# Optimization experiments

Hardware: AMD Instinct MI355X
Metric: run time of the kernel (lower is better)

## Reference

```python
import jax, jax.numpy as jnp
import numpy as np

B, S, H = 4, 2048, 1024
E, K, F = 8, 2, 4096


def setup_inputs() -> dict:
    key = jax.random.key(0)
    ks = jax.random.split(key, 6)
    x = jax.random.normal(ks[0], (B, S, H), dtype=jnp.float32)
    gate_w = jax.random.normal(ks[1], (H, E), dtype=jnp.float32) * 0.02
    w1 = jax.random.normal(ks[2], (E, H, F), dtype=jnp.float32) * 0.02
    b1 = jnp.zeros((E, F), dtype=jnp.float32)
    w2 = jax.random.normal(ks[3], (E, F, H), dtype=jnp.float32) * 0.02
    b2 = jnp.zeros((E, H), dtype=jnp.float32)
    return {"x": x, "gate_w": gate_w, "w1": w1, "b1": b1, "w2": w2, "b2": b2}


def reference(x, gate_w, w1, b1, w2, b2):
    # NOTE: the torch module masks expert inputs per token, but since each
    # expert's output is re-masked by the same mask, the math is exactly
    # out[t] = sum_i renorm_prob[t,i] * expert_{topk_idx[t,i]}(x[t]).
    # Dropout is identity in eval mode.
    T = B * S
    x_flat = x.reshape(T, H)

    gate_scores = x_flat @ gate_w                      # [T, E]
    gate_probs = jax.nn.softmax(gate_scores, axis=-1)  # [T, E]
    topk_vals, topk_idx = jax.lax.top_k(gate_probs, K)  # [T, K]
    topk_w = jax.nn.softmax(topk_vals, axis=-1)        # renormalize via softmax (as in source)

    # Combine weights per (token, expert): sum over top-k slots.
    onehot = jax.nn.one_hot(topk_idx, E, dtype=x.dtype)           # [T, K, E]
    comb = jnp.einsum('tk,tke->te', topk_w, onehot)               # [T, E]

    # Run all experts densely (faithful to naive module; combine masks out unrouted).
    h = jnp.einsum('th,ehf->etf', x_flat, w1) + b1[:, None, :]    # [E, T, F]
    h = jax.nn.relu(h)
    expert_out = jnp.einsum('etf,efh->eth', h, w2) + b2[:, None, :]  # [E, T, H]

    out_flat = jnp.einsum('te,eth->th', comb, expert_out)         # [T, H]
    output = out_flat.reshape(B, S, H)

    # Load-balance loss: KL(uniform || softmax(mean gate prob)), batchmean over E.
    expert_usage = gate_probs.mean(axis=0)                        # [E]
    log_sm = jax.nn.log_softmax(expert_usage, axis=0)
    uniform = jnp.full((E,), 1.0 / E, dtype=x.dtype)
    kl = jnp.sum(uniform * (jnp.log(uniform) - log_sm)) / E
    load_balance_loss = 0.01 * kl
    return output, load_balance_loss
```

## Files before the change

kernel.cpp:

```cpp
#include <hip/hip_runtime.h>
#include <stdint.h>

#define T_TOK 8192
#define HD 1024
#define NE 8
#define FD 4096
#define RALLOC 18432
#define G1 1152
#define G2 384
#define NKT1 16
#define GATE_BLOCKS 1024

typedef __attribute__((ext_vector_type(8))) short bf16x8;
typedef __attribute__((ext_vector_type(4))) float f32x4;
typedef __attribute__((ext_vector_type(4))) short s16x4;

__device__ __forceinline__ unsigned short f2bf(float f) {
  unsigned u = __builtin_bit_cast(unsigned, f);
  u += 0x7fffu + ((u >> 16) & 1u);
  return (unsigned short)(u >> 16);
}

__device__ __forceinline__ void gld_lds16(const void* g, void* l) {
  __builtin_amdgcn_global_load_lds(
      (const __attribute__((address_space(1))) void*)g,
      (__attribute__((address_space(3))) void*)l, 16, 0, 0);
}

__global__ __launch_bounds__(256) void k_transpose2(const float* __restrict__ w1,
                                                    const float* __restrict__ w2,
                                                    unsigned short* __restrict__ w1t,
                                                    unsigned short* __restrict__ w2t) {
  __shared__ unsigned short tile[64 * 80];
  const int i = blockIdx.x;
  const float* src;
  unsigned short* dst;
  int R, C, r0, c0;
  if (i < 8192) {
    const int e = i >> 10, rem = i & 1023;
    R = HD; C = FD; r0 = (rem >> 6) << 6; c0 = (rem & 63) << 6;
    src = w1 + (size_t)e * R * C; dst = w1t + (size_t)e * R * C;
  } else {
    const int e = (i - 8192) >> 10, rem = (i - 8192) & 1023;
    R = FD; C = HD; r0 = (rem >> 4) << 6; c0 = (rem & 15) << 6;
    src = w2 + (size_t)e * R * C; dst = w2t + (size_t)e * R * C;
  }
  const int tid = threadIdx.x;
  {
    const int r = tid >> 2, cg = (tid & 3) * 16;
    #pragma unroll
    for (int m = 0; m < 4; ++m) {
      float4 v = *(const float4*)(src + (size_t)(r0 + r) * C + c0 + cg + 4 * m);
      s16x4 pv;
      pv[0] = (short)f2bf(v.x); pv[1] = (short)f2bf(v.y);
      pv[2] = (short)f2bf(v.z); pv[3] = (short)f2bf(v.w);
      *(s16x4*)&tile[r * 80 + cg + 4 * m] = pv;
    }
  }
  __syncthreads();
  {
    const int c = tid >> 2, rg = (tid & 3) * 16;
    bf16x8 v0, v1;
    #pragma unroll
    for (int j = 0; j < 8; ++j) v0[j] = (short)tile[(rg + j) * 80 + c];
    #pragma unroll
    for (int j = 0; j < 8; ++j) v1[j] = (short)tile[(rg + 8 + j) * 80 + c];
    unsigned short* dp = dst + (size_t)(c0 + c) * R + r0 + rg;
    *(bf16x8*)dp = v0;
    *(bf16x8*)(dp + 8) = v1;
  }
}

__global__ __launch_bounds__(512) void k_gating(const float* __restrict__ x,
                                                const float* __restrict__ gw,
                                                int* __restrict__ toke,
                                                float* __restrict__ tokw,
                                                int* __restrict__ counts8,
                                                double* __restrict__ part,
                                                unsigned short* __restrict__ xbf) {
  __shared__ float gwT[8 * 1024];
  __shared__ double sp[8][8];
  __shared__ int scnt[8];
  const int tid = threadIdx.x;
  const int lane = tid & 63;
  const int w = tid >> 6;
  if (tid < 8) scnt[tid] = 0;
  #pragma unroll
  for (int rep = 0; rep < 16; ++rep) {
    int idx = rep * 512 + tid;
    gwT[(idx & 7) * 1024 + (idx >> 3)] = gw[idx];
  }
  __syncthreads();

  const int t = blockIdx.x * 8 + w;
  double acc[8];
  #pragma unroll
  for (int e = 0; e < 8; ++e) acc[e] = 0.0;
  const float* xr = x + (size_t)t * HD;
  unsigned short* xbr = xbf + (size_t)t * HD;
  #pragma unroll
  for (int j = 0; j < 4; ++j) {
    const int hh = j * 256 + lane * 4;
    float4 xv = *(const float4*)(xr + hh);
    s16x4 pv;
    pv[0] = (short)f2bf(xv.x); pv[1] = (short)f2bf(xv.y);
    pv[2] = (short)f2bf(xv.z); pv[3] = (short)f2bf(xv.w);
    *(s16x4*)(xbr + hh) = pv;
    #pragma unroll
    for (int e = 0; e < 8; ++e) {
      float4 gv = *(const float4*)(gwT + e * 1024 + hh);
      acc[e] += (double)xv.x * (double)gv.x;
      acc[e] += (double)xv.y * (double)gv.y;
      acc[e] += (double)xv.z * (double)gv.z;
      acc[e] += (double)xv.w * (double)gv.w;
    }
  }
  for (int off = 32; off > 0; off >>= 1) {
    #pragma unroll
    for (int e = 0; e < 8; ++e) acc[e] += __shfl_xor(acc[e], off, 64);
  }
  double m = acc[0];
  #pragma unroll
  for (int e = 1; e < 8; ++e) m = fmax(m, acc[e]);
  double p[8], ssum = 0.0;
  #pragma unroll
  for (int e = 0; e < 8; ++e) { p[e] = exp(acc[e] - m); ssum += p[e]; }
  double inv = 1.0 / ssum;
  #pragma unroll
  for (int e = 0; e < 8; ++e) p[e] *= inv;
  int e0 = 0;
  #pragma unroll
  for (int e = 1; e < 8; ++e) if (p[e] > p[e0]) e0 = e;
  int e1 = (e0 == 0) ? 1 : 0;
  #pragma unroll
  for (int e = 0; e < 8; ++e) if (e != e0 && p[e] > p[e1]) e1 = e;
  if (lane == 0) {
    double z = exp(p[e1] - p[e0]);
    double w0 = 1.0 / (1.0 + z);
    toke[2 * t] = e0; toke[2 * t + 1] = e1;
    tokw[2 * t] = (float)w0; tokw[2 * t + 1] = (float)(z / (1.0 + z));
    atomicAdd(&scnt[e0], 1);
    atomicAdd(&scnt[e1], 1);
    #pragma unroll
    for (int e = 0; e < 8; ++e) sp[w][e] = p[e];
  }
  __syncthreads();
  if (tid < 8) {
    double s = 0.0;
    #pragma unroll
    for (int q = 0; q < 8; ++q) s += sp[q][tid];
    part[(size_t)blockIdx.x * 8 + tid] = s;
    counts8[(size_t)blockIdx.x * 8 + tid] = scnt[tid];
  }
}

__global__ __launch_bounds__(256) void k_scan(const int* __restrict__ counts8,
                                              int* __restrict__ offs,
                                              int* __restrict__ cursors,
                                              const double* __restrict__ part,
                                              float* __restrict__ loss_out,
                                              int* __restrict__ rowmap,
                                              float* __restrict__ roww) {
  __shared__ double su[8];
  __shared__ int soffs[9];
  __shared__ int scnt[8];
  const int tid = threadIdx.x;
  const int e = tid >> 5, sub = tid & 31;
  double s = 0.0;
  int c = 0;
  for (int b = sub; b < GATE_BLOCKS; b += 32) {
    s += part[(size_t)b * 8 + e];
    c += counts8[(size_t)b * 8 + e];
  }
  for (int off = 16; off > 0; off >>= 1) {
    s += __shfl_xor(s, off, 64);
    c += __shfl_xor(c, off, 64);
  }
  if (sub == 0) { su[e] = s; scnt[e] = c; }
  __syncthreads();
  if (tid == 0) {
    int o = 0;
    for (int i = 0; i < 8; ++i) {
      soffs[i] = o; offs[i] = o; cursors[i * 16] = o;
      o += ((scnt[i] + 255) >> 8) << 8;
    }
    soffs[8] = o; offs[8] = o;
    double u[8], mx = -1e300;
    for (int i = 0; i < 8; ++i) { u[i] = su[i] / 8192.0; mx = fmax(mx, u[i]); }
    double se = 0.0;
    for (int i = 0; i < 8; ++i) se += exp(u[i] - mx);
    double lse = mx + log(se);
    double kl = 0.0;
    const double lu = log(0.125);
    for (int i = 0; i < 8; ++i) kl += 0.125 * (lu - (u[i] - lse));
    kl /= 8.0;
    loss_out[0] = (float)(0.01 * kl);
  }
  __syncthreads();
  for (int i = 0; i < 8; ++i) {
    int s0 = soffs[i] + scnt[i];
    int en = soffs[i + 1];
    for (int k = s0 + tid; k < en; k += 256) { rowmap[k] = 2 * T_TOK; roww[k] = 0.f; }
  }
}

__global__ __launch_bounds__(256) void k_scatter(const int* __restrict__ toke,
                                                 const float* __restrict__ tokw,
                                                 int* __restrict__ cursors,
                                                 int* __restrict__ rowmap,
                                                 float* __restrict__ roww) {
  const int t = blockIdx.x * 256 + threadIdx.x;
  const int lane = threadIdx.x & 63;
  #pragma unroll
  for (int k = 0; k < 2; ++k) {
    int e = toke[2 * t + k];
    float wv = tokw[2 * t + k];
    for (int ex = 0; ex < 8; ++ex) {
      unsigned long long mask = __ballot(e == ex);
      if (e == ex) {
        int leader = __ffsll((unsigned long long)mask) - 1;
        int rank = __popcll(mask & ((1ull << lane) - 1ull));
        int base = 0;
        if (lane == leader) base = atomicAdd(&cursors[ex * 16], __popcll(mask));
        base = __shfl(base, leader, 64);
        rowmap[base + rank] = 2 * t + k;
        roww[base + rank] = wv;
      }
    }
  }
}

#define RDA(buf, mh) do { _Pragma("unroll") for (int m_ = 0; m_ < 4; ++m_) { \
  af[m_][0] = *(const bf16x8*)(lds + (buf) * 65536 + wmOff + (mh) * 8192 + aoff[m_][0]); \
  af[m_][1] = *(const bf16x8*)(lds + (buf) * 65536 + wmOff + (mh) * 8192 + aoff[m_][1]); } } while (0)

#define RDB(buf, nh, B) do { _Pragma("unroll") for (int nf_ = 0; nf_ < 2; ++nf_) { \
  B[nf_][0] = *(const bf16x8*)(lds + (buf) * 65536 + wnOff + (nh) * 4096 + boff[nf_][0]); \
  B[nf_][1] = *(const bf16x8*)(lds + (buf) * 65536 + wnOff + (nh) * 4096 + boff[nf_][1]); } } while (0)

#define MMA(mh, nh, B) do { _Pragma("unroll") for (int m_ = 0; m_ < 4; ++m_) \
  _Pragma("unroll") for (int nf_ = 0; nf_ < 2; ++nf_) \
  _Pragma("unroll") for (int kh_ = 0; kh_ < 2; ++kh_) \
    acc[(mh) * 4 + m_][(nh) * 2 + nf_] = __builtin_amdgcn_mfma_f32_16x16x32_bf16( \
        af[m_][kh_], B[nf_][kh_], acc[(mh) * 4 + m_][(nh) * 2 + nf_], 0, 0, 0); } while (0)

#define SYNC_PRE() do { __builtin_amdgcn_sched_barrier(0); __builtin_amdgcn_s_barrier(); \
  asm volatile("s_waitcnt lgkmcnt(0)" ::: "memory"); __builtin_amdgcn_sched_barrier(0); \
  __builtin_amdgcn_s_setprio(1); } while (0)

#define SYNC_POST() do { __builtin_amdgcn_s_setprio(0); __builtin_amdgcn_sched_barrier(0); \
  __builtin_amdgcn_s_barrier(); __builtin_amdgcn_sched_barrier(0); } while (0)

#define SYNC_POST_VM() do { __builtin_amdgcn_s_setprio(0); __builtin_amdgcn_sched_barrier(0); \
  asm volatile("s_waitcnt vmcnt(4)" ::: "memory"); __builtin_amdgcn_sched_barrier(0); \
  __builtin_amdgcn_s_barrier(); __builtin_amdgcn_sched_barrier(0); } while (0)

#define FRAG_OFFSETS256() \
  int aoff[4][2], boff[2][2]; \
  { \
    const int kg = (lane >> 4) << 4; \
    _Pragma("unroll") \
    for (int m = 0; m < 4; ++m) { \
      int r = m * 16 + (lane & 15); \
      _Pragma("unroll") \
      for (int kh = 0; kh < 2; ++kh) \
        aoff[m][kh] = r * 128 + ((kh * 64 + kg) ^ ((r & 7) << 4)); \
    } \
    _Pragma("unroll") \
    for (int nf = 0; nf < 2; ++nf) { \
      int r = (wn & 1) * 64 + nf * 16 + (lane & 15); \
      _Pragma("unroll") \
      for (int kh = 0; kh < 2; ++kh) \
        boff[nf][kh] = r * 128 + ((kh * 64 + kg) ^ ((r & 7) << 4)); \
    } \
  }

__global__ __launch_bounds__(512, 2) void k_gemm1(const unsigned short* __restrict__ xbf,
                                                  const unsigned short* __restrict__ w1t,
                                                  const float* __restrict__ b1,
                                                  const int* __restrict__ rowmap,
                                                  const int* __restrict__ offs,
                                                  unsigned short* __restrict__ hbuf) {
  __shared__ char lds[131072];
  const int id = blockIdx.x;
  const int xcd = id & 7, l = id >> 3;
  const int ntr = offs[8] >> 8;
  const int nj = ntr * 16;
  const int q = nj >> 3, r8 = nj & 7;
  const int cnt = q + (xcd < r8 ? 1 : 0);
  if (l >= cnt) return;
  const int start = (xcd < r8) ? xcd * (q + 1) : r8 * (q + 1) + (xcd - r8) * q;
  const int g = start + l;
  const int rt = g >> 4, nb = g & 15;
  const int row0 = rt * 256;
  int e = 0;
  #pragma unroll
  for (int i = 1; i < 8; ++i) if (row0 >= offs[i]) e = i;
  const int n0 = nb * 256;
  const int tid = threadIdx.x;
  const int lane = tid & 63;
  const int wid = tid >> 6;
  const int wm = wid >> 2, wn = wid & 3;

  const int rl = tid >> 3;
  const int cbs = ((tid & 7) << 4) ^ ((rl & 7) << 4);
  const char* pA[2][2];
  #pragma unroll
  for (int h = 0; h < 2; ++h)
    #pragma unroll
    for (int l2 = 0; l2 < 2; ++l2) {
      int tok = rowmap[row0 + h * 128 + l2 * 64 + rl] >> 1;
      pA[h][l2] = (const char*)xbf + (size_t)tok * 2048 + cbs;
    }
  const char* pB00 = (const char*)w1t + (size_t)e * ((size_t)FD * HD * 2) +
                     (size_t)(n0 + rl) * 2048 + cbs;
  const int stw = wid * 1024;

#define STA1(buf, h, kt) do { \
  gld_lds16(pA[h][0] + (size_t)(kt) * 128, lds + (buf) * 65536 + (h) * 16384 + stw); \
  gld_lds16(pA[h][1] + (size_t)(kt) * 128, lds + (buf) * 65536 + (h) * 16384 + 8192 + stw); } while (0)
#define STB1(buf, h, kt) do { \
  gld_lds16(pB00 + (size_t)(h) * 128 * 2048 + (size_t)(kt) * 128, \
            lds + (buf) * 65536 + 32768 + (h) * 16384 + stw); \
  gld_lds16(pB00 + ((size_t)(h) * 128 + 64) * 2048 + (size_t)(kt) * 128, \
            lds + (buf) * 65536 + 32768 + (h) * 16384 + 8192 + stw); } while (0)

  FRAG_OFFSETS256();
  const int wmOff = wm * 16384;
  const int wnOff = 32768 + (wn >> 1) * 16384;

  f32x4 acc[8][4];
  #pragma unroll
  for (int a = 0; a < 8; ++a)
    #pragma unroll
    for (int b = 0; b < 4; ++b) acc[a][b] = (f32x4){0.f, 0.f, 0.f, 0.f};
  bf16x8 af[4][2], b0r[2][2], b1r[2][2];

  STA1(0, 0, 0); STA1(0, 1, 0); STB1(0, 0, 0); STB1(0, 1, 0);
  STB1(1, 0, 1); STB1(1, 1, 1);
  asm volatile("s_waitcnt vmcnt(4)" ::: "memory");
  __builtin_amdgcn_sched_barrier(0);
  __builtin_amdgcn_s_barrier();
  __builtin_amdgcn_sched_barrier(0);

  #pragma unroll 1
  for (int i = 0; i < NKT1 / 2; ++i) {
    const int k1 = 2 * i + 1, k2 = 2 * i + 2, k3 = 2 * i + 3;
    RDA(0, 0); RDB(0, 0, b0r); STA1(1, 0, k1); SYNC_PRE(); MMA(0, 0, b0r); SYNC_POST();
    RDB(0, 1, b1r);            STA1(1, 1, k1); SYNC_PRE(); MMA(0, 1, b1r); SYNC_POST();
    RDA(0, 1);                 STB1(0, 0, k2); SYNC_PRE(); MMA(1, 1, b1r); SYNC_POST();
                               STB1(0, 1, k2); SYNC_PRE(); MMA(1, 0, b0r); SYNC_POST_VM();
    RDA(1, 0); RDB(1, 0, b0r); STA1(0, 0, k2); SYNC_PRE(); MMA(0, 0, b0r); SYNC_POST();
    RDB(1, 1, b1r);            STA1(0, 1, k2); SYNC_PRE(); MMA(0, 1, b1r); SYNC_POST();
    RDA(1, 1);                 STB1(1, 0, k3); SYNC_PRE(); MMA(1, 1, b1r); SYNC_POST();
                               STB1(1, 1, k3); SYNC_PRE(); MMA(1, 0, b0r); SYNC_POST_VM();
  }

  asm volatile("s_waitcnt vmcnt(0)" ::: "memory");
  __builtin_amdgcn_sched_barrier(0);
  __syncthreads();
  #pragma unroll
  for (int na = 0; na < 4; ++na) {
    int c = wn * 64 + (na >> 1) * 32 + (na & 1) * 16 + (lane & 15);
    float bias = b1[(size_t)e * FD + n0 + c];
    #pragma unroll
    for (int ma = 0; ma < 8; ++ma) {
      #pragma unroll
      for (int j2 = 0; j2 < 4; ++j2) {
        int r = wm * 128 + (ma >> 2) * 64 + (ma & 3) * 16 + ((lane >> 4) << 2) + j2;
        float v = fmaxf(acc[ma][na][j2] + bias, 0.f);
        *(unsigned short*)(lds + r * 512 + ((c * 2) ^ ((r & 7) << 4))) = f2bf(v);
      }
    }
  }
  __syncthreads();
  #pragma unroll
  for (int s = 0; s < 16; ++s) {
    int flat = s * 512 + tid;
    int r = flat >> 5, ch = flat & 31;
    bf16x8 v = *(const bf16x8*)(lds + r * 512 + ((ch * 16) ^ ((r & 7) << 4)));
    *(bf16x8*)((char*)hbuf + (size_t)(row0 + r) * 8192 + (size_t)n0 * 2 + ch * 16) = v;
  }
#undef STA1
#undef STB1
}

__global__ __launch_bounds__(512, 2) void k_gemm2(const unsigned short* __restrict__ hbuf,
                                                  const unsigned short* __restrict__ w2t,
                                                  const float* __restrict__ b2,
                                                  const int* __restrict__ rowmap,
                                                  const float* __restrict__ roww,
                                                  const int* __restrict__ offs,
                                                  float* __restrict__ out2,
                                                  float* __restrict__ psplit) {
  __shared__ char lds[131072];
  const int id = blockIdx.x;
  int bx, by, kt0, niter, jj = -1;
  if (id < 256) {
    const int sid = (id & 7) * 32 + (id >> 3);
    bx = sid & 3; by = sid >> 2;
    kt0 = 0; niter = 32;
  } else {
    const int jid = id - 256;
    const int q = (jid & 7) * 16 + (jid >> 3);
    const int t = 256 + (q >> 2);
    const int nT2 = (offs[8] >> 8) * 4;
    if (t >= nT2) return;
    bx = t & 3; by = t >> 2;
    kt0 = (q & 3) * 16; niter = 8;
    jj = q;
  }
  const int row0 = by * 256;
  int e = 0;
  #pragma unroll
  for (int i = 1; i < 8; ++i) if (row0 >= offs[i]) e = i;
  const int n0 = bx * 256;
  const int tid = threadIdx.x;
  const int lane = tid & 63;
  const int wid = tid >> 6;
  const int wm = wid >> 2, wn = wid & 3;

  const int rl = tid >> 3;
  const int cbs = ((tid & 7) << 4) ^ ((rl & 7) << 4);
  const char* pA00 = (const char*)hbuf + (size_t)(row0 + rl) * 8192 + cbs;
  const char* pB00 = (const char*)w2t + (size_t)e * ((size_t)HD * FD * 2) +
                     (size_t)(n0 + rl) * 8192 + cbs;
  const int stw = wid * 1024;

#define STA2(buf, h, kt) do { \
  gld_lds16(pA00 + (size_t)(h) * 128 * 8192 + (size_t)(kt) * 128, \
            lds + (buf) * 65536 + (h) * 16384 + stw); \
  gld_lds16(pA00 + ((size_t)(h) * 128 + 64) * 8192 + (size_t)(kt) * 128, \
            lds + (buf) * 65536 + (h) * 16384 + 8192 + stw); } while (0)
#define STB2(buf, h, kt) do { \
  gld_lds16(pB00 + (size_t)(h) * 128 * 8192 + (size_t)(kt) * 128, \
            lds + (buf) * 65536 + 32768 + (h) * 16384 + stw); \
  gld_lds16(pB00 + ((size_t)(h) * 128 + 64) * 8192 + (size_t)(kt) * 128, \
            lds + (buf) * 65536 + 32768 + (h) * 16384 + 8192 + stw); } while (0)

  FRAG_OFFSETS256();
  const int wmOff = wm * 16384;
  const int wnOff = 32768 + (wn >> 1) * 16384;

  f32x4 acc[8][4];
  #pragma unroll
  for (int a = 0; a < 8; ++a)
    #pragma unroll
    for (int b = 0; b < 4; ++b) acc[a][b] = (f32x4){0.f, 0.f, 0.f, 0.f};
  bf16x8 af[4][2], b0r[2][2], b1r[2][2];

  STA2(0, 0, kt0); STA2(0, 1, kt0); STB2(0, 0, kt0); STB2(0, 1, kt0);
  STB2(1, 0, kt0 + 1); STB2(1, 1, kt0 + 1);
  asm volatile("s_waitcnt vmcnt(4)" ::: "memory");
  __builtin_amdgcn_sched_barrier(0);
  __builtin_amdgcn_s_barrier();
  __builtin_amdgcn_sched_barrier(0);

  #pragma unroll 1
  for (int i = 0; i < niter; ++i) {
    const int k1 = kt0 + 2 * i + 1, k2 = kt0 + 2 * i + 2, k3 = kt0 + 2 * i + 3;
    RDA(0, 0); RDB(0, 0, b0r); STA2(1, 0, k1); SYNC_PRE(); MMA(0, 0, b0r); SYNC_POST();
    RDB(0, 1, b1r);            STA2(1, 1, k1); SYNC_PRE(); MMA(0, 1, b1r); SYNC_POST();
    RDA(0, 1);                 STB2(0, 0, k2); SYNC_PRE(); MMA(1, 1, b1r); SYNC_POST();
                               STB2(0, 1, k2); SYNC_PRE(); MMA(1, 0, b0r); SYNC_POST_VM();
    RDA(1, 0); RDB(1, 0, b0r); STA2(0, 0, k2); SYNC_PRE(); MMA(0, 0, b0r); SYNC_POST();
    RDB(1, 1, b1r);            STA2(0, 1, k2); SYNC_PRE(); MMA(0, 1, b1r); SYNC_POST();
    RDA(1, 1);                 STB2(1, 0, k3); SYNC_PRE(); MMA(1, 1, b1r); SYNC_POST();
                               STB2(1, 1, k3); SYNC_PRE(); MMA(1, 0, b0r); SYNC_POST_VM();
  }

  asm volatile("s_waitcnt vmcnt(0)" ::: "memory");
  __builtin_amdgcn_sched_barrier(0);
  if (jj < 0) {
    #pragma unroll
    for (int ma = 0; ma < 8; ++ma) {
      #pragma unroll
      for (int j2 = 0; j2 < 4; ++j2) {
        int r = wm * 128 + (ma >> 2) * 64 + (ma & 3) * 16 + ((lane >> 4) << 2) + j2;
        int rm = rowmap[row0 + r];
        float wr = roww[row0 + r];
        float* orow = out2 + (size_t)rm * 1024 + n0;
        #pragma unroll
        for (int na = 0; na < 4; ++na) {
          int c = wn * 64 + (na >> 1) * 32 + (na & 1) * 16 + (lane & 15);
          orow[c] = (acc[ma][na][j2] + b2[(size_t)e * HD + n0 + c]) * wr;
        }
      }
    }
  } else {
    float* ps = psplit + (size_t)jj * 65536;
    #pragma unroll
    for (int ma = 0; ma < 8; ++ma) {
      #pragma unroll
      for (int j2 = 0; j2 < 4; ++j2) {
        int r = wm * 128 + (ma >> 2) * 64 + (ma & 3) * 16 + ((lane >> 4) << 2) + j2;
        #pragma unroll
        for (int na = 0; na < 4; ++na) {
          int c = wn * 64 + (na >> 1) * 32 + (na & 1) * 16 + (lane & 15);
          ps[r * 256 + c] = acc[ma][na][j2];
        }
      }
    }
  }
#undef STA2
#undef STB2
}

__global__ __launch_bounds__(512) void k_fix2(const float* __restrict__ psplit,
                                              const int* __restrict__ offs,
                                              const float* __restrict__ b2,
                                              const int* __restrict__ rowmap,
                                              const float* __restrict__ roww,
                                              float* __restrict__ out2) {
  const int nT2 = (offs[8] >> 8) * 4;
  const int t = 256 + blockIdx.x;
  if (t >= nT2) return;
  const int by = t >> 2, bx = t & 3;
  const int row0 = by * 256, n0 = bx * 256;
  int e = 0;
  #pragma unroll
  for (int i = 1; i < 8; ++i) if (row0 >= offs[i]) e = i;
  const float* ps = psplit + (size_t)blockIdx.x * 4 * 65536;
  const int cg = (threadIdx.x & 63) * 4;
  const int r0t = threadIdx.x >> 6;
  float4 bb = *(const float4*)(b2 + (size_t)e * HD + n0 + cg);
  for (int rr = 0; rr < 32; ++rr) {
    int r = rr * 8 + r0t;
    int rm = rowmap[row0 + r];
    float wr = roww[row0 + r];
    float4 s0 = *(const float4*)(ps + 0 * 65536 + r * 256 + cg);
    float4 s1 = *(const float4*)(ps + 1 * 65536 + r * 256 + cg);
    float4 s2 = *(const float4*)(ps + 2 * 65536 + r * 256 + cg);
    float4 s3 = *(const float4*)(ps + 3 * 65536 + r * 256 + cg);
    float4 o;
    o.x = wr * (s0.x + s1.x + s2.x + s3.x + bb.x);
    o.y = wr * (s0.y + s1.y + s2.y + s3.y + bb.y);
    o.z = wr * (s0.z + s1.z + s2.z + s3.z + bb.z);
    o.w = wr * (s0.w + s1.w + s2.w + s3.w + bb.w);
    *(float4*)(out2 + (size_t)rm * 1024 + n0 + cg) = o;
  }
}

__global__ __launch_bounds__(256) void k_combine(const float* __restrict__ out2,
                                                 float* __restrict__ out) {
  const int t = blockIdx.x;
  const int i = threadIdx.x * 4;
  float4 a = *(const float4*)(out2 + (size_t)(2 * t) * 1024 + i);
  float4 b = *(const float4*)(out2 + (size_t)(2 * t + 1) * 1024 + i);
  float4 r;
  r.x = a.x + b.x; r.y = a.y + b.y; r.z = a.z + b.z; r.w = a.w + b.w;
  *(float4*)(out + (size_t)t * 1024 + i) = r;
}

extern "C" void kernel_launch(void* const* d_in, const int* in_sizes, int n_in,
                              void* d_out, int out_size, void* d_ws, size_t ws_size,
                              hipStream_t stream) {
  const float* x = (const float*)d_in[0];
  const float* gw = (const float*)d_in[1];
  const float* w1 = (const float*)d_in[2];
  const float* b1 = (const float*)d_in[3];
  const float* w2 = (const float*)d_in[4];
  const float* b2 = (const float*)d_in[5];
  float* out = (float*)d_out;

  char* ws = (char*)d_ws;
  size_t o = 0;
  unsigned short* w2t = (unsigned short*)(ws + o); o += (size_t)NE * HD * FD * 2;
  unsigned short* hbuf = (unsigned short*)(ws + o); o += (size_t)RALLOC * FD * 2;
  unsigned short* w1t = (unsigned short*)(ws + o);
  size_t w1t_off = o; o += (size_t)NE * FD * HD * 2;
  unsigned short* xbf = (unsigned short*)(ws + o); o += (size_t)T_TOK * HD * 2;
  int* rowmap = (int*)(ws + o); o += (size_t)RALLOC * 4;
  float* roww = (float*)(ws + o); o += (size_t)RALLOC * 4;
  int* toke = (int*)(ws + o); o += (size_t)T_TOK * 2 * 4;
  float* tokw = (float*)(ws + o); o += (size_t)T_TOK * 2 * 4;
  double* part = (double*)(ws + o); o += (size_t)GATE_BLOCKS * 8 * 8;
  int* counts8 = (int*)(ws + o); o += (size_t)GATE_BLOCKS * 8 * 4;
  int* ctrl = (int*)(ws + o); o += 1024;
  int* offs = ctrl;
  int* cursors = ctrl + 64;
  float* psplit = (float*)(ws + o); o += (size_t)128 * 65536 * 4;
  float* out2 = (float*)(ws + w1t_off);

  k_transpose2<<<16384, 256, 0, stream>>>(w1, w2, w1t, w2t);
  k_gating<<<GATE_BLOCKS, 512, 0, stream>>>(x, gw, toke, tokw, counts8, part, xbf);
  k_scan<<<1, 256, 0, stream>>>(counts8, offs, cursors, part, out + (size_t)T_TOK * HD,
                                rowmap, roww);
  k_scatter<<<T_TOK / 256, 256, 0, stream>>>(toke, tokw, cursors, rowmap, roww);
  k_gemm1<<<G1, 512, 0, stream>>>(xbf, w1t, b1, rowmap, offs, hbuf);
  k_gemm2<<<G2, 512, 0, stream>>>(hbuf, w2t, b2, rowmap, roww, offs, out2, psplit);
  k_fix2<<<32, 512, 0, stream>>>(psplit, offs, b2, rowmap, roww, out2);
  k_combine<<<T_TOK, 256, 0, stream>>>(out2, out);
}
```

Measured before the change: 469.5 us.

## Fold w2 transpose into gemm1 launch as extra blocks to overlap

Splits the weight transpose kernel so only w1 is converted up front. The w2 fp32-to-bf16 transpose is moved into extra blocks appended to the gemm1 grid, two tiles per 512-thread block. The intent is to hide the w2 conversion's memory traffic behind gemm1's compute instead of running it serially. The extra blocks share the gemm1 kernel's 128KB LDS footprint and launch bounds, which may limit how many of them run at once and could delay gemm1 blocks.

```diff
diff --git a/kernel.cpp b/kernel.cpp
--- a/kernel.cpp
+++ b/kernel.cpp
@@ -27,24 +27,15 @@
       (__attribute__((address_space(3))) void*)l, 16, 0, 0);
 }
 
-__global__ __launch_bounds__(256) void k_transpose2(const float* __restrict__ w1,
-                                                    const float* __restrict__ w2,
-                                                    unsigned short* __restrict__ w1t,
-                                                    unsigned short* __restrict__ w2t) {
+__global__ __launch_bounds__(256) void k_transpose1(const float* __restrict__ w1,
+                                                    unsigned short* __restrict__ w1t) {
   __shared__ unsigned short tile[64 * 80];
   const int i = blockIdx.x;
-  const float* src;
-  unsigned short* dst;
-  int R, C, r0, c0;
-  if (i < 8192) {
-    const int e = i >> 10, rem = i & 1023;
-    R = HD; C = FD; r0 = (rem >> 6) << 6; c0 = (rem & 63) << 6;
-    src = w1 + (size_t)e * R * C; dst = w1t + (size_t)e * R * C;
-  } else {
-    const int e = (i - 8192) >> 10, rem = (i - 8192) & 1023;
-    R = FD; C = HD; r0 = (rem >> 4) << 6; c0 = (rem & 15) << 6;
-    src = w2 + (size_t)e * R * C; dst = w2t + (size_t)e * R * C;
-  }
+  const int e = i >> 10, rem = i & 1023;
+  const int R = HD, C = FD;
+  const int r0 = (rem >> 6) << 6, c0 = (rem & 63) << 6;
+  const float* src = w1 + (size_t)e * R * C;
+  unsigned short* dst = w1t + (size_t)e * R * C;
   const int tid = threadIdx.x;
   {
     const int r = tid >> 2, cg = (tid & 3) * 16;
@@ -280,9 +271,47 @@
                                                   const float* __restrict__ b1,
                                                   const int* __restrict__ rowmap,
                                                   const int* __restrict__ offs,
-                                                  unsigned short* __restrict__ hbuf) {
+                                                  unsigned short* __restrict__ hbuf,
+                                                  const float* __restrict__ w2,
+                                                  unsigned short* __restrict__ w2t) {
   __shared__ char lds[131072];
   const int id = blockIdx.x;
+  const int tid = threadIdx.x;
+  if (id >= G1) {
+    const int half = tid >> 8;
+    const int t2 = tid & 255;
+    unsigned short* tile = (unsigned short*)(lds + half * 10240);
+    const int tt = (id - G1) * 2 + half;
+    const int e = tt >> 10, rem = tt & 1023;
+    const int R = FD, C = HD;
+    const int r0 = (rem >> 4) << 6, c0 = (rem & 15) << 6;
+    const float* src = w2 + (size_t)e * R * C;
+    unsigned short* dst = w2t + (size_t)e * R * C;
+    {
+      const int r = t2 >> 2, cg = (t2 & 3) * 16;
+      #pragma unroll
+      for (int m = 0; m < 4; ++m) {
+        float4 v = *(const float4*)(src + (size_t)(r0 + r) * C + c0 + cg + 4 * m);
+        s16x4 pv;
+        pv[0] = (short)f2bf(v.x); pv[1] = (short)f2bf(v.y);
+        pv[2] = (short)f2bf(v.z); pv[3] = (short)f2bf(v.w);
+        *(s16x4*)&tile[r * 80 + cg + 4 * m] = pv;
+      }
+    }
+    __syncthreads();
+    {
+      const int c = t2 >> 2, rg = (t2 & 3) * 16;
+      bf16x8 v0, v1;
+      #pragma unroll
+      for (int j = 0; j < 8; ++j) v0[j] = (short)tile[(rg + j) * 80 + c];
+      #pragma unroll
+      for (int j = 0; j < 8; ++j) v1[j] = (short)tile[(rg + 8 + j) * 80 + c];
+      unsigned short* dp = dst + (size_t)(c0 + c) * R + r0 + rg;
+      *(bf16x8*)dp = v0;
+      *(bf16x8*)(dp + 8) = v1;
+    }
+    return;
+  }
   const int xcd = id & 7, l = id >> 3;
   const int ntr = offs[8] >> 8;
   const int nj = ntr * 16;
@@ -297,7 +326,6 @@
   #pragma unroll
   for (int i = 1; i < 8; ++i) if (row0 >= offs[i]) e = i;
   const int n0 = nb * 256;
-  const int tid = threadIdx.x;
   const int lane = tid & 63;
   const int wid = tid >> 6;
   const int wm = wid >> 2, wn = wid & 3;
@@ -582,12 +610,12 @@
   float* psplit = (float*)(ws + o); o += (size_t)128 * 65536 * 4;
   float* out2 = (float*)(ws + w1t_off);
 
-  k_transpose2<<<16384, 256, 0, stream>>>(w1, w2, w1t, w2t);
+  k_transpose1<<<8192, 256, 0, stream>>>(w1, w1t);
   k_gating<<<GATE_BLOCKS, 512, 0, stream>>>(x, gw, toke, tokw, counts8, part, xbf);
   k_scan<<<1, 256, 0, stream>>>(counts8, offs, cursors, part, out + (size_t)T_TOK * HD,
                                 rowmap, roww);
   k_scatter<<<T_TOK / 256, 256, 0, stream>>>(toke, tokw, cursors, rowmap, roww);
-  k_gemm1<<<G1, 512, 0, stream>>>(xbf, w1t, b1, rowmap, offs, hbuf);
+  k_gemm1<<<G1 + 4096, 512, 0, stream>>>(xbf, w1t, b1, rowmap, offs, hbuf, w2, w2t);
   k_gemm2<<<G2, 512, 0, stream>>>(hbuf, w2t, b2, rowmap, roww, offs, out2, psplit);
   k_fix2<<<32, 512, 0, stream>>>(psplit, offs, b2, rowmap, roww, out2);
   k_combine<<<T_TOK, 256, 0, stream>>>(out2, out);
```

Measured after the change: 456.3 us. 1.03x faster.
